# Kernel optimization log

Measured on AMD Instinct MI355X. Metric: run time of the kernel, lower is better.

## Reference

```python
import jax, jax.numpy as jnp
import numpy as np


def log_g(x):
    # log of g(x) where g(x) = x + 0.5 for x >= 0 else sigmoid(x)
    return jnp.where(x >= 0, jnp.log(jnp.where(x >= 0, x, 0.0) + 0.5), -jax.nn.softplus(-x))


def mingru_layer(x, h0, W, b):
    # x: (B,S,Din), h0: (B,1,H) positive, W: (2H,Din), b: (2H,)
    gh = jnp.einsum('bsd,ed->bse', x, W) + b
    gate, hidden = jnp.split(gh, 2, axis=-1)
    log_z = -jax.nn.softplus(-gate)        # log sigmoid(gate)
    log_coeffs = -jax.nn.softplus(gate)    # log (1 - sigmoid(gate))
    log_values = jnp.concatenate([jnp.log(h0), log_z + log_g(hidden)], axis=1)  # (B,S+1,H)
    a_star = jnp.pad(jnp.cumsum(log_coeffs, axis=1), ((0, 0), (1, 0), (0, 0)))  # (B,S+1,H)
    log_h = a_star + jax.lax.cumlogsumexp(log_values - a_star, axis=1)
    return jnp.exp(log_h)[:, 1:]  # (B,S,H)


def setup_inputs() -> dict:
    key = jax.random.key(0)
    ks = jax.random.split(key, 6)
    B, S, D, H = 8, 2048, 1024, 1024
    L = 2
    s = 0.02
    return {
        'x': jax.random.normal(ks[0], (B, S, D), jnp.float32),
        'h': jax.random.uniform(ks[1], (L, B, 1, H), jnp.float32, 0.05, 1.0),
        'w0': jax.random.normal(ks[2], (2 * H, D), jnp.float32) * s,
        'b0': jax.random.normal(ks[3], (2 * H,), jnp.float32) * s,
        'w1': jax.random.normal(ks[4], (2 * H, H), jnp.float32) * s,
        'b1': jax.random.normal(ks[5], (2 * H,), jnp.float32) * s,
    }


def reference(x, h, w0, b0, w1, b1):
    # layer 0 (residual, align = Identity since input_dims == hidden_dims)
    out0 = mingru_layer(x, h[0], w0, b0)
    h0_final = out0[:, -1:]
    inp = out0 + x
    # layer 1 (last layer: residual, no dropout after)
    out1 = mingru_layer(inp, h[1], w1, b1)
    h1_final = out1[:, -1:]
    out = out1 + inp
    h_final = jnp.stack([h0_final, h1_final])  # (L,B,1,H)
    return out, h_final
```

## Files before the change

### kernel.cpp

```cpp
#include <hip/hip_runtime.h>
#include <hip/hip_bf16.h>
#include <cstdint>
#include <cstddef>

#define GAS __attribute__((address_space(1)))
#define LAS __attribute__((address_space(3)))

typedef __attribute__((ext_vector_type(8))) __bf16 bf16x8;
typedef __attribute__((ext_vector_type(4))) float f32x4;

constexpr int kB = 8, kS = 2048, kK = 1024, kH = 1024;
constexpr int kM = kB * kS;
constexpr int kN2 = 2 * kH;
constexpr int BM = 256, BN = 256, BK = 32;
constexpr int NKT = kK / BK;

constexpr size_t kOffXb   = 0;
constexpr size_t kOffW0   = 33554432;
constexpr size_t kOffW1   = 37748736;
constexpr size_t kOffA    = 41943040;
constexpr size_t kOffG    = 75497472;
constexpr size_t kOffCA   = 109051904;
constexpr size_t kOffCV   = 111149056;
constexpr size_t kOffHst  = 113246208;
constexpr size_t kWsNeed  = 115343360;

__device__ __forceinline__ ushort f2bf(float f) {
    union { float f; uint32_t u; } v; v.f = f;
    uint32_t r = v.u + 0x7FFFu + ((v.u >> 16) & 1u);
    return (ushort)(r >> 16);
}
__device__ __forceinline__ float bf2f(ushort u) {
    union { uint32_t u; float f; } v; v.u = (uint32_t)u << 16;
    return v.f;
}

__global__ void cvt_bf16_kernel(const float* __restrict__ src, ushort* __restrict__ dst, int n4) {
    int i = blockIdx.x * blockDim.x + threadIdx.x;
    if (i >= n4) return;
    f32x4 v = *reinterpret_cast<const f32x4*>(src + (size_t)i * 4);
    ushort4 o;
    o.x = f2bf(v.x); o.y = f2bf(v.y); o.z = f2bf(v.z); o.w = f2bf(v.w);
    *reinterpret_cast<ushort4*>(dst + (size_t)i * 4) = o;
}

__global__ __launch_bounds__(512, 1)
void gemm_scan_kernel(const ushort* __restrict__ A, const ushort* __restrict__ W,
                      const float* __restrict__ bias,
                      ushort* __restrict__ Apref, ushort* __restrict__ Vpref,
                      float* __restrict__ cA, float* __restrict__ cV)
{
    __shared__ ushort smem[69632];

    const int tid  = threadIdx.x;
    const int lane = tid & 63;
    const int wv   = tid >> 6;
    const int wm   = wv >> 2;
    const int wn   = wv & 3;

    const int bid = blockIdx.x;
    const int sid = (bid & 7) * 64 + (bid >> 3);
    const int tm  = sid >> 3;
    const int tn  = sid & 7;
    const int m0  = tm * BM;
    const int j0  = tn * 128;

    f32x4 acc[8][4];
#pragma unroll
    for (int i = 0; i < 8; ++i)
#pragma unroll
        for (int j = 0; j < 4; ++j) acc[i][j] = (f32x4){0.f, 0.f, 0.f, 0.f};

    const int srow  = wv * 16 + (lane >> 2);
    const int sslot = (lane & 3) ^ ((lane >> 3) & 3);
    const int scol  = sslot * 8;

    const ushort* ga0 = A + (size_t)(m0 + srow) * kK + scol;
    const ushort* ga1 = ga0 + (size_t)128 * kK;
    const ushort* gb0 = W + (size_t)(j0 + srow) * kK + scol;
    const ushort* gb1 = W + (size_t)(1024 + j0 + srow) * kK + scol;

    char* lds = (char*)smem;
    const int ldsw = wv * 1024;

    const int rslot = (lane >> 4) ^ ((lane >> 1) & 3);
    const int rb    = (lane & 15) * 64 + rslot * 16;
    const int aoff  = wm * 8192 + rb;
    const int boff  = 16384 + wn * 4096 + rb;

#define VMWAIT(N) asm volatile("s_waitcnt vmcnt(" #N ")" ::: "memory")

#define STAGE_A(SBUF) do {                                                       \
    __builtin_amdgcn_global_load_lds((const GAS void*)(ga0),                     \
        (LAS void*)(lds + (SBUF) * 32768 + ldsw),          16, 0, 0);            \
    __builtin_amdgcn_global_load_lds((const GAS void*)(ga1),                     \
        (LAS void*)(lds + (SBUF) * 32768 + 8192  + ldsw),  16, 0, 0);            \
  } while (0)

#define STAGE_B(SBUF) do {                                                       \
    __builtin_amdgcn_global_load_lds((const GAS void*)(gb0),                     \
        (LAS void*)(lds + (SBUF) * 32768 + 16384 + ldsw),  16, 0, 0);            \
    __builtin_amdgcn_global_load_lds((const GAS void*)(gb1),                     \
        (LAS void*)(lds + (SBUF) * 32768 + 24576 + ldsw),  16, 0, 0);            \
    ga0 += BK; ga1 += BK; gb0 += BK; gb1 += BK;                                  \
  } while (0)

#define TILE_GEN(BUF, SA, SB, EW) do {                                           \
    bf16x8 bf_[4], af_[4];                                                       \
    _Pragma("unroll")                                                            \
    for (int nf_ = 0; nf_ < 4; ++nf_)                                            \
        bf_[nf_] = *reinterpret_cast<const bf16x8*>(                             \
            lds + (BUF) * 32768 + boff + nf_ * 1024);                            \
    _Pragma("unroll")                                                            \
    for (int mf_ = 0; mf_ < 4; ++mf_)                                            \
        af_[mf_] = *reinterpret_cast<const bf16x8*>(                             \
            lds + (BUF) * 32768 + aoff + mf_ * 1024);                            \
    SA;                                                                          \
    __builtin_amdgcn_s_barrier();                                                \
    asm volatile("s_waitcnt lgkmcnt(0)" ::: "memory");                           \
    __builtin_amdgcn_sched_barrier(0);                                           \
    __builtin_amdgcn_s_setprio(1);                                               \
    _Pragma("unroll")                                                            \
    for (int mf_ = 0; mf_ < 4; ++mf_)                                            \
        _Pragma("unroll")                                                        \
        for (int nf_ = 0; nf_ < 4; ++nf_)                                        \
            acc[mf_][nf_] = __builtin_amdgcn_mfma_f32_16x16x32_bf16(             \
                af_[mf_], bf_[nf_], acc[mf_][nf_], 0, 0, 0);                     \
    __builtin_amdgcn_s_setprio(0);                                               \
    __builtin_amdgcn_s_barrier();                                                \
    _Pragma("unroll")                                                            \
    for (int mf_ = 0; mf_ < 4; ++mf_)                                            \
        af_[mf_] = *reinterpret_cast<const bf16x8*>(                             \
            lds + (BUF) * 32768 + aoff + 4096 + mf_ * 1024);                     \
    SB;                                                                          \
    __builtin_amdgcn_s_barrier();                                                \
    asm volatile("s_waitcnt lgkmcnt(0)" ::: "memory");                           \
    __builtin_amdgcn_sched_barrier(0);                                           \
    __builtin_amdgcn_s_setprio(1);                                               \
    _Pragma("unroll")                                                            \
    for (int mf_ = 0; mf_ < 4; ++mf_)                                            \
        _Pragma("unroll")                                                        \
        for (int nf_ = 0; nf_ < 4; ++nf_)                                        \
            acc[4 + mf_][nf_] = __builtin_amdgcn_mfma_f32_16x16x32_bf16(         \
                af_[mf_], bf_[nf_], acc[4 + mf_][nf_], 0, 0, 0);                 \
    __builtin_amdgcn_s_setprio(0);                                               \
    EW;                                                                          \
    __builtin_amdgcn_s_barrier();                                                \
  } while (0)

#define TILE(BUF, SBUF) TILE_GEN(BUF, STAGE_A(SBUF), STAGE_B(SBUF), VMWAIT(4))
#define TAIL0(BUF)      TILE_GEN(BUF, (void)0, (void)0, VMWAIT(0))
#define TAIL1(BUF)      TILE_GEN(BUF, (void)0, (void)0, (void)0)

    STAGE_A(0); STAGE_B(0);
    STAGE_A(1); STAGE_B(1);
    VMWAIT(4);
    __builtin_amdgcn_s_barrier();

    for (int g = 0; g < 7; ++g) {
        TILE(0, 2);
        TILE(1, 3);
        TILE(2, 0);
        TILE(3, 1);
    }
    TILE(0, 2);
    TILE(1, 3);
    TAIL0(2);
    TAIL1(3);

#undef TILE
#undef TAIL0
#undef TAIL1
#undef TILE_GEN
#undef STAGE_A
#undef STAGE_B
#undef VMWAIT

    ushort* a_lds = smem;
    ushort* g_lds = smem + 33792;
    float*  sumA  = (float*)(smem + 67584);
    float*  sumV  = sumA + 512;

    {
        const bool isG = (wn < 2);
        ushort* tgt = isG ? a_lds : g_lds;
        const int jl = (wn & 1) * 64;
        float bn[4];
#pragma unroll
        for (int nf = 0; nf < 4; ++nf)
            bn[nf] = bias[(isG ? 0 : 1024) + j0 + jl + nf * 16 + (lane & 15)];
#pragma unroll
        for (int mf = 0; mf < 8; ++mf) {
#pragma unroll
            for (int i = 0; i < 4; ++i) {
                const int m = wm * 128 + mf * 16 + (lane >> 4) * 4 + i;
#pragma unroll
                for (int nf = 0; nf < 4; ++nf) {
                    float val = acc[mf][nf][i] + bn[nf];
                    float r;
                    if (isG) r = 1.f / (1.f + __expf(val));
                    else     r = (val >= 0.f) ? val + 0.5f : 1.f / (1.f + __expf(-val));
                    tgt[m * 132 + jl + nf * 16 + (lane & 15)] = f2bf(r);
                }
            }
        }
    }
    __syncthreads();

    {
        const int j  = tid & 127;
        const int sg = tid >> 7;
        float A1 = 1.f, V1 = 0.f;
#pragma unroll 4
        for (int t = 0; t < 64; ++t) {
            const int s = sg * 64 + t;
            float a = bf2f(a_lds[s * 132 + j]);
            float g = bf2f(g_lds[s * 132 + j]);
            V1 = a * V1 + (1.f - a) * g;
            A1 *= a;
        }
        sumA[sg * 128 + j] = A1;
        sumV[sg * 128 + j] = V1;
        __syncthreads();
        float Ar = 1.f, Vr = 0.f;
        for (int k = 0; k < sg; ++k) {
            float Ak = sumA[k * 128 + j], Vk = sumV[k * 128 + j];
            Vr = Ak * Vr + Vk;
            Ar *= Ak;
        }
        ushort* ApG = Apref + (size_t)(m0 + sg * 64) * kH + j0 + j;
        ushort* VpG = Vpref + (size_t)(m0 + sg * 64) * kH + j0 + j;
#pragma unroll 4
        for (int t = 0; t < 64; ++t) {
            const int s = sg * 64 + t;
            float a = bf2f(a_lds[s * 132 + j]);
            float g = bf2f(g_lds[s * 132 + j]);
            Vr = a * Vr + (1.f - a) * g;
            Ar *= a;
            *ApG = f2bf(Ar);
            *VpG = f2bf(Vr);
            ApG += kH; VpG += kH;
        }
        if (sg == 3) {
            const int b = tm >> 3, c = tm & 7;
            cA[((b * 8 + c) << 10) + j0 + j] = Ar;
            cV[((b * 8 + c) << 10) + j0 + j] = Vr;
        }
    }
}

__global__ void scan_chunks_kernel(const float* __restrict__ cA, const float* __restrict__ cV,
                                   const float* __restrict__ h0, float* __restrict__ hstart,
                                   float* __restrict__ hfin)
{
    int idx = blockIdx.x * 256 + threadIdx.x;
    int j = idx & 1023, b = idx >> 10;
    float h = h0[(b << 10) + j];
    for (int c = 0; c < 8; ++c) {
        int o = ((b * 8 + c) << 10) + j;
        hstart[o] = h;
        h = cA[o] * h + cV[o];
    }
    hfin[(b << 10) + j] = h;
}

template<bool WRITE_F32>
__global__ void apply_kernel(const ushort* __restrict__ Ap, const ushort* __restrict__ Vp,
                             const float* __restrict__ hst, const ushort* __restrict__ res,
                             void* __restrict__ outp)
{
    size_t i = ((size_t)blockIdx.x * 256 + threadIdx.x) * 4;
    int m = (int)(i >> 10);
    int j = (int)(i & 1023);
    int b = m >> 11, s = m & 2047, c = s >> 8;
    f32x4 hcs = *reinterpret_cast<const f32x4*>(hst + (((b * 8 + c) << 10) + j));
    ushort4 Au = *reinterpret_cast<const ushort4*>(Ap + i);
    ushort4 Vu = *reinterpret_cast<const ushort4*>(Vp + i);
    ushort4 Ru = *reinterpret_cast<const ushort4*>(res + i);
    f32x4 o;
    o.x = bf2f(Au.x) * hcs.x + bf2f(Vu.x) + bf2f(Ru.x);
    o.y = bf2f(Au.y) * hcs.y + bf2f(Vu.y) + bf2f(Ru.y);
    o.z = bf2f(Au.z) * hcs.z + bf2f(Vu.z) + bf2f(Ru.z);
    o.w = bf2f(Au.w) * hcs.w + bf2f(Vu.w) + bf2f(Ru.w);
    if (WRITE_F32) {
        *reinterpret_cast<f32x4*>((float*)outp + i) = o;
    } else {
        ushort4 ob;
        ob.x = f2bf(o.x); ob.y = f2bf(o.y); ob.z = f2bf(o.z); ob.w = f2bf(o.w);
        *reinterpret_cast<ushort4*>((ushort*)outp + i) = ob;
    }
}

extern "C" void kernel_launch(void* const* d_in, const int* in_sizes, int n_in,
                              void* d_out, int out_size, void* d_ws, size_t ws_size,
                              hipStream_t stream)
{
    const float* x  = (const float*)d_in[0];
    const float* h  = (const float*)d_in[1];
    const float* w0 = (const float*)d_in[2];
    const float* b0 = (const float*)d_in[3];
    const float* w1 = (const float*)d_in[4];
    const float* b1 = (const float*)d_in[5];
    float* out = (float*)d_out;
    char* ws = (char*)d_ws;

    if (ws_size < kWsNeed) return;

    ushort* xb   = (ushort*)(ws + kOffXb);
    ushort* inpb = (ushort*)(ws + kOffXb);
    ushort* w0b  = (ushort*)(ws + kOffW0);
    ushort* w1b  = (ushort*)(ws + kOffW1);
    ushort* Ap   = (ushort*)(ws + kOffA);
    ushort* Vp   = (ushort*)(ws + kOffG);
    float*  cA   = (float*)(ws + kOffCA);
    float*  cV   = (float*)(ws + kOffCV);
    float*  hst  = (float*)(ws + kOffHst);

    float* out_h = out + (size_t)kM * kH;

    cvt_bf16_kernel<<<(kM * kK / 4 + 255) / 256, 256, 0, stream>>>(x, xb, kM * kK / 4);
    cvt_bf16_kernel<<<(kN2 * kK / 4 + 255) / 256, 256, 0, stream>>>(w0, w0b, kN2 * kK / 4);
    cvt_bf16_kernel<<<(kN2 * kK / 4 + 255) / 256, 256, 0, stream>>>(w1, w1b, kN2 * kK / 4);

    const int gemm_grid  = (kM / BM) * (kN2 / BN);
    const int apply_grid = kM * kH / 4 / 256;

    gemm_scan_kernel<<<gemm_grid, 512, 0, stream>>>(xb, w0b, b0, Ap, Vp, cA, cV);
    scan_chunks_kernel<<<32, 256, 0, stream>>>(cA, cV, h, hst, out_h);
    apply_kernel<false><<<apply_grid, 256, 0, stream>>>(Ap, Vp, hst, xb, inpb);

    gemm_scan_kernel<<<gemm_grid, 512, 0, stream>>>(inpb, w1b, b1, Ap, Vp, cA, cV);
    scan_chunks_kernel<<<32, 256, 0, stream>>>(cA, cV, h + (size_t)kB * kH, hst, out_h + (size_t)kB * kH);
    apply_kernel<true><<<apply_grid, 256, 0, stream>>>(Ap, Vp, hst, inpb, out);
}
```

Before: 272.1 us.

## Fuse GEMM, chunk scan and apply into one persistent cooperative kernel

Replaces the per-layer GEMM+scan, chunk-scan and apply kernels with a single cooperative kernel of 256 persistent blocks. Each block computes two row tiles per layer and uses grid.sync to exchange per-chunk carry values. It then re-runs the recurrence from the gate tiles still held in shared memory and writes the output directly. This removes the global bf16 prefix arrays Ap/Vp, the hstart buffer and several kernel launches. In exchange it adds four grid-wide barriers, a serial carry loop over previous chunks in each block, and a dependence on all 256 blocks being co-resident.

```diff
diff --git a/kernel.cpp b/kernel.cpp
--- a/kernel.cpp
+++ b/kernel.cpp
@@ -1,8 +1,11 @@
 #include <hip/hip_runtime.h>
+#include <hip/hip_cooperative_groups.h>
 #include <hip/hip_bf16.h>
 #include <cstdint>
 #include <cstddef>
 
+namespace cg = cooperative_groups;
+
 #define GAS __attribute__((address_space(1)))
 #define LAS __attribute__((address_space(3)))
 
@@ -12,18 +15,15 @@
 constexpr int kB = 8, kS = 2048, kK = 1024, kH = 1024;
 constexpr int kM = kB * kS;
 constexpr int kN2 = 2 * kH;
-constexpr int BM = 256, BN = 256, BK = 32;
+constexpr int BM = 256, BK = 32;
 constexpr int NKT = kK / BK;
 
-constexpr size_t kOffXb   = 0;
-constexpr size_t kOffW0   = 33554432;
-constexpr size_t kOffW1   = 37748736;
-constexpr size_t kOffA    = 41943040;
-constexpr size_t kOffG    = 75497472;
-constexpr size_t kOffCA   = 109051904;
-constexpr size_t kOffCV   = 111149056;
-constexpr size_t kOffHst  = 113246208;
-constexpr size_t kWsNeed  = 115343360;
+constexpr size_t kOffXb  = 0;
+constexpr size_t kOffW0  = 33554432;
+constexpr size_t kOffW1  = 37748736;
+constexpr size_t kOffCA  = 41943040;
+constexpr size_t kOffCV  = 42205184;
+constexpr size_t kWsNeed = 42467328;
 
 __device__ __forceinline__ ushort f2bf(float f) {
     union { float f; uint32_t u; } v; v.f = f;
@@ -44,26 +44,19 @@
     *reinterpret_cast<ushort4*>(dst + (size_t)i * 4) = o;
 }
 
-__global__ __launch_bounds__(512, 1)
-void gemm_scan_kernel(const ushort* __restrict__ A, const ushort* __restrict__ W,
-                      const float* __restrict__ bias,
-                      ushort* __restrict__ Apref, ushort* __restrict__ Vpref,
-                      float* __restrict__ cA, float* __restrict__ cV)
+__device__ __forceinline__ void do_tile(const ushort* __restrict__ Ain,
+                                        const ushort* __restrict__ Wt,
+                                        const float* __restrict__ bias,
+                                        ushort* smem, int m0, int j0, int tid,
+                                        float* __restrict__ cA, float* __restrict__ cV,
+                                        int b, int c)
 {
-    __shared__ ushort smem[69632];
-
-    const int tid  = threadIdx.x;
     const int lane = tid & 63;
     const int wv   = tid >> 6;
     const int wm   = wv >> 2;
     const int wn   = wv & 3;
 
-    const int bid = blockIdx.x;
-    const int sid = (bid & 7) * 64 + (bid >> 3);
-    const int tm  = sid >> 3;
-    const int tn  = sid & 7;
-    const int m0  = tm * BM;
-    const int j0  = tn * 128;
+    __syncthreads();
 
     f32x4 acc[8][4];
 #pragma unroll
@@ -75,14 +68,13 @@
     const int sslot = (lane & 3) ^ ((lane >> 3) & 3);
     const int scol  = sslot * 8;
 
-    const ushort* ga0 = A + (size_t)(m0 + srow) * kK + scol;
+    const ushort* ga0 = Ain + (size_t)(m0 + srow) * kK + scol;
     const ushort* ga1 = ga0 + (size_t)128 * kK;
-    const ushort* gb0 = W + (size_t)(j0 + srow) * kK + scol;
-    const ushort* gb1 = W + (size_t)(1024 + j0 + srow) * kK + scol;
+    const ushort* gb0 = Wt + (size_t)(j0 + srow) * kK + scol;
+    const ushort* gb1 = Wt + (size_t)(1024 + j0 + srow) * kK + scol;
 
     char* lds = (char*)smem;
     const int ldsw = wv * 1024;
-
     const int rslot = (lane >> 4) ^ ((lane >> 1) & 3);
     const int rb    = (lane & 15) * 64 + rslot * 16;
     const int aoff  = wm * 8192 + rb;
@@ -180,7 +172,6 @@
     ushort* g_lds = smem + 33792;
     float*  sumA  = (float*)(smem + 67584);
     float*  sumV  = sumA + 512;
-
     {
         const bool isG = (wn < 2);
         ushort* tgt = isG ? a_lds : g_lds;
@@ -222,73 +213,90 @@
         sumA[sg * 128 + j] = A1;
         sumV[sg * 128 + j] = V1;
         __syncthreads();
-        float Ar = 1.f, Vr = 0.f;
-        for (int k = 0; k < sg; ++k) {
-            float Ak = sumA[k * 128 + j], Vk = sumV[k * 128 + j];
-            Vr = Ak * Vr + Vk;
-            Ar *= Ak;
-        }
-        ushort* ApG = Apref + (size_t)(m0 + sg * 64) * kH + j0 + j;
-        ushort* VpG = Vpref + (size_t)(m0 + sg * 64) * kH + j0 + j;
-#pragma unroll 4
-        for (int t = 0; t < 64; ++t) {
-            const int s = sg * 64 + t;
-            float a = bf2f(a_lds[s * 132 + j]);
-            float g = bf2f(g_lds[s * 132 + j]);
-            Vr = a * Vr + (1.f - a) * g;
-            Ar *= a;
-            *ApG = f2bf(Ar);
-            *VpG = f2bf(Vr);
-            ApG += kH; VpG += kH;
-        }
-        if (sg == 3) {
-            const int b = tm >> 3, c = tm & 7;
+        if (sg == 0) {
+            float Ar = 1.f, Vr = 0.f;
+#pragma unroll
+            for (int k = 0; k < 4; ++k) {
+                float Ak = sumA[k * 128 + j], Vk = sumV[k * 128 + j];
+                Vr = Ak * Vr + Vk;
+                Ar *= Ak;
+            }
             cA[((b * 8 + c) << 10) + j0 + j] = Ar;
             cV[((b * 8 + c) << 10) + j0 + j] = Vr;
         }
     }
 }
 
-__global__ void scan_chunks_kernel(const float* __restrict__ cA, const float* __restrict__ cV,
-                                   const float* __restrict__ h0, float* __restrict__ hstart,
-                                   float* __restrict__ hfin)
+template<bool WRITE_F32>
+__device__ __forceinline__ void do_apply(ushort* smem, int m0, int j0, int tid,
+    const float* __restrict__ cA, const float* __restrict__ cV,
+    const float* __restrict__ h0L, const ushort* __restrict__ res,
+    void* __restrict__ outp, float* __restrict__ outhL, int b, int c)
 {
-    int idx = blockIdx.x * 256 + threadIdx.x;
-    int j = idx & 1023, b = idx >> 10;
-    float h = h0[(b << 10) + j];
-    for (int c = 0; c < 8; ++c) {
-        int o = ((b * 8 + c) << 10) + j;
-        hstart[o] = h;
-        h = cA[o] * h + cV[o];
-    }
-    hfin[(b << 10) + j] = h;
-}
-
-template<bool WRITE_F32>
-__global__ void apply_kernel(const ushort* __restrict__ Ap, const ushort* __restrict__ Vp,
-                             const float* __restrict__ hst, const ushort* __restrict__ res,
-                             void* __restrict__ outp)
+    ushort* a_lds = smem;
+    ushort* g_lds = smem + 33792;
+    float*  sumA  = (float*)(smem + 67584);
+    float*  sumV  = sumA + 512;
+    const int j  = tid & 127;
+    const int sg = tid >> 7;
+
+    float hv = h0L[(b << 10) + j0 + j];
+    for (int k = 0; k < c; ++k) {
+        int o = ((b * 8 + k) << 10) + j0 + j;
+        hv = cA[o] * hv + cV[o];
+    }
+    for (int k = 0; k < sg; ++k)
+        hv = sumA[k * 128 + j] * hv + sumV[k * 128 + j];
+
+    const size_t gbase = (size_t)(m0 + sg * 64) * kH + j0 + j;
+    const ushort* rp = res + gbase;
+#pragma unroll 4
+    for (int t = 0; t < 64; ++t) {
+        const int s = sg * 64 + t;
+        float a = bf2f(a_lds[s * 132 + j]);
+        float g = bf2f(g_lds[s * 132 + j]);
+        hv = a * hv + (1.f - a) * g;
+        float o = hv + bf2f(*rp);
+        if (WRITE_F32) ((float*)outp)[gbase + (size_t)t * kH] = o;
+        else           ((ushort*)outp)[gbase + (size_t)t * kH] = f2bf(o);
+        rp += kH;
+    }
+    if (c == 7 && sg == 3) outhL[(b << 10) + j0 + j] = hv;
+}
+
+__global__ __launch_bounds__(512, 1)
+void fused_mingru_kernel(ushort* xb,
+                         const ushort* w0b, const ushort* w1b,
+                         const float* b0, const float* b1,
+                         const float* h0,
+                         float* cA, float* cV,
+                         float* out)
 {
-    size_t i = ((size_t)blockIdx.x * 256 + threadIdx.x) * 4;
-    int m = (int)(i >> 10);
-    int j = (int)(i & 1023);
-    int b = m >> 11, s = m & 2047, c = s >> 8;
-    f32x4 hcs = *reinterpret_cast<const f32x4*>(hst + (((b * 8 + c) << 10) + j));
-    ushort4 Au = *reinterpret_cast<const ushort4*>(Ap + i);
-    ushort4 Vu = *reinterpret_cast<const ushort4*>(Vp + i);
-    ushort4 Ru = *reinterpret_cast<const ushort4*>(res + i);
-    f32x4 o;
-    o.x = bf2f(Au.x) * hcs.x + bf2f(Vu.x) + bf2f(Ru.x);
-    o.y = bf2f(Au.y) * hcs.y + bf2f(Vu.y) + bf2f(Ru.y);
-    o.z = bf2f(Au.z) * hcs.z + bf2f(Vu.z) + bf2f(Ru.z);
-    o.w = bf2f(Au.w) * hcs.w + bf2f(Vu.w) + bf2f(Ru.w);
-    if (WRITE_F32) {
-        *reinterpret_cast<f32x4*>((float*)outp + i) = o;
-    } else {
-        ushort4 ob;
-        ob.x = f2bf(o.x); ob.y = f2bf(o.y); ob.z = f2bf(o.z); ob.w = f2bf(o.w);
-        *reinterpret_cast<ushort4*>((ushort*)outp + i) = ob;
-    }
+    __shared__ ushort smem[69632];
+    cg::grid_group grid = cg::this_grid();
+
+    const int tid = threadIdx.x;
+    const int k   = blockIdx.x;
+    const int j0  = (k & 7) * 128;
+    const int tmA = k >> 3;
+    const int tmB = 32 + (k >> 3);
+
+    float* out_h = out + (size_t)kM * kH;
+    const float* h1 = h0 + 8192;
+
+    do_tile(xb, w0b, b0, smem, tmA * BM, j0, tid, cA, cV, tmA >> 3, tmA & 7);
+    grid.sync();
+    do_apply<false>(smem, tmA * BM, j0, tid, cA, cV, h0, xb, (void*)xb, out_h, tmA >> 3, tmA & 7);
+    do_tile(xb, w0b, b0, smem, tmB * BM, j0, tid, cA, cV, tmB >> 3, tmB & 7);
+    grid.sync();
+    do_apply<false>(smem, tmB * BM, j0, tid, cA, cV, h0, xb, (void*)xb, out_h, tmB >> 3, tmB & 7);
+
+    do_tile(xb, w1b, b1, smem, tmA * BM, j0, tid, cA, cV, tmA >> 3, tmA & 7);
+    grid.sync();
+    do_apply<true>(smem, tmA * BM, j0, tid, cA, cV, h1, xb, (void*)out, out_h + 8192, tmA >> 3, tmA & 7);
+    do_tile(xb, w1b, b1, smem, tmB * BM, j0, tid, cA, cV, tmB >> 3, tmB & 7);
+    grid.sync();
+    do_apply<true>(smem, tmB * BM, j0, tid, cA, cV, h1, xb, (void*)out, out_h + 8192, tmB >> 3, tmB & 7);
 }
 
 extern "C" void kernel_launch(void* const* d_in, const int* in_sizes, int n_in,
@@ -306,30 +314,20 @@
 
     if (ws_size < kWsNeed) return;
 
-    ushort* xb   = (ushort*)(ws + kOffXb);
-    ushort* inpb = (ushort*)(ws + kOffXb);
-    ushort* w0b  = (ushort*)(ws + kOffW0);
-    ushort* w1b  = (ushort*)(ws + kOffW1);
-    ushort* Ap   = (ushort*)(ws + kOffA);
-    ushort* Vp   = (ushort*)(ws + kOffG);
-    float*  cA   = (float*)(ws + kOffCA);
-    float*  cV   = (float*)(ws + kOffCV);
-    float*  hst  = (float*)(ws + kOffHst);
-
-    float* out_h = out + (size_t)kM * kH;
+    ushort* xb  = (ushort*)(ws + kOffXb);
+    ushort* w0b = (ushort*)(ws + kOffW0);
+    ushort* w1b = (ushort*)(ws + kOffW1);
+    float*  cA  = (float*)(ws + kOffCA);
+    float*  cV  = (float*)(ws + kOffCV);
 
     cvt_bf16_kernel<<<(kM * kK / 4 + 255) / 256, 256, 0, stream>>>(x, xb, kM * kK / 4);
     cvt_bf16_kernel<<<(kN2 * kK / 4 + 255) / 256, 256, 0, stream>>>(w0, w0b, kN2 * kK / 4);
     cvt_bf16_kernel<<<(kN2 * kK / 4 + 255) / 256, 256, 0, stream>>>(w1, w1b, kN2 * kK / 4);
 
-    const int gemm_grid  = (kM / BM) * (kN2 / BN);
-    const int apply_grid = kM * kH / 4 / 256;
-
-    gemm_scan_kernel<<<gemm_grid, 512, 0, stream>>>(xb, w0b, b0, Ap, Vp, cA, cV);
-    scan_chunks_kernel<<<32, 256, 0, stream>>>(cA, cV, h, hst, out_h);
-    apply_kernel<false><<<apply_grid, 256, 0, stream>>>(Ap, Vp, hst, xb, inpb);
-
-    gemm_scan_kernel<<<gemm_grid, 512, 0, stream>>>(inpb, w1b, b1, Ap, Vp, cA, cV);
-    scan_chunks_kernel<<<32, 256, 0, stream>>>(cA, cV, h + (size_t)kB * kH, hst, out_h + (size_t)kB * kH);
-    apply_kernel<true><<<apply_grid, 256, 0, stream>>>(Ap, Vp, hst, inpb, out);
-}
+    const ushort* w0bc = w0b; const ushort* w1bc = w1b;
+    const float*  b0c = b0;  const float*  b1c = b1;  const float* hc = h;
+    void* args[] = { (void*)&xb, (void*)&w0bc, (void*)&w1bc, (void*)&b0c, (void*)&b1c,
+                     (void*)&hc, (void*)&cA, (void*)&cV, (void*)&out };
+    hipLaunchCooperativeKernel((const void*)fused_mingru_kernel,
+                               dim3(256), dim3(512), args, 0, stream);
+}
```

Result: slower. 355.8 us (+30.8%).
